# Performance work log

Measured on AMD Instinct MI355X. Metric: run time of the kernel, lower is better.

## Reference

```python
import jax, jax.numpy as jnp
import numpy as np

B, S, D, H = 2, 2048, 2048, 16
HD = D // H  # head_dim = 128


def setup_inputs() -> dict:
    key = jax.random.key(0)
    ks = jax.random.split(key, 5)
    scale = 1.0 / np.sqrt(D)
    return {
        "x": jax.random.normal(ks[0], (B, S, D), dtype=jnp.float32),
        "wq": jax.random.normal(ks[1], (D, D), dtype=jnp.float32) * scale,
        "wk": jax.random.normal(ks[2], (D, D), dtype=jnp.float32) * scale,
        "wv": jax.random.normal(ks[3], (D, D), dtype=jnp.float32) * scale,
        "wo": jax.random.normal(ks[4], (D, D), dtype=jnp.float32) * scale,
        "bo": jnp.zeros((D,), dtype=jnp.float32),
    }


def reference(x, wq, wk, wv, wo, bo):
    b, s, _ = x.shape
    # torch Linear: y = x @ W.T ; then view(b,s,H,HD) and transpose to (b,H,s,HD)
    q = (x @ wq.T).reshape(b, s, H, HD).transpose(0, 2, 1, 3)
    k = (x @ wk.T).reshape(b, s, H, HD).transpose(0, 2, 1, 3)
    v = (x @ wv.T).reshape(b, s, H, HD).transpose(0, 2, 1, 3)
    scores = jnp.einsum("bhqd,bhkd->bhqk", q, k)
    causal = jnp.triu(jnp.ones((s, s), dtype=bool), k=1)  # True above diagonal
    scores = jnp.where(causal[None, None], -jnp.inf, scores)
    attn = jax.nn.softmax(scores / np.sqrt(HD), axis=-1)
    # dropout p=0.0 -> identity
    ctx = jnp.einsum("bhqk,bhkd->bhqd", attn, v)
    ctx = ctx.transpose(0, 2, 1, 3).reshape(b, s, D)
    return ctx @ wo.T + bo
```

## Files before the change

kernel.cpp:

```cpp
#include <hip/hip_runtime.h>
#include <math.h>

typedef __bf16 bf16_t;
typedef __bf16 bf16x8 __attribute__((ext_vector_type(8)));
typedef float f32x4 __attribute__((ext_vector_type(4)));

__device__ __forceinline__ void gload_lds16(const bf16_t* g, bf16_t* l) {
    __builtin_amdgcn_global_load_lds((const __attribute__((address_space(1))) void*)g,
                                     (__attribute__((address_space(3))) void*)l, 16, 0, 0);
}

__global__ __launch_bounds__(256) void cvt_all(const float* __restrict__ x,
                                               const float* __restrict__ wq,
                                               const float* __restrict__ wk,
                                               const float* __restrict__ wv,
                                               const float* __restrict__ wo,
                                               bf16_t* __restrict__ dst) {
    int c = blockIdx.x * 256 + threadIdx.x;
    const float* src;
    size_t off;
    if (c < 1048576) { src = x; off = c; }
    else {
        int q = (c - 1048576) >> 19;
        src = (q == 0) ? wq : (q == 1) ? wk : (q == 2) ? wv : wo;
        off = (c - 1048576) & 524287;
    }
    const float4* p = (const float4*)src + off * 2;
    float4 a = p[0], b = p[1];
    union { bf16_t h[8]; uint4 u; } pk;
    pk.h[0] = (bf16_t)a.x; pk.h[1] = (bf16_t)a.y; pk.h[2] = (bf16_t)a.z; pk.h[3] = (bf16_t)a.w;
    pk.h[4] = (bf16_t)b.x; pk.h[5] = (bf16_t)b.y; pk.h[6] = (bf16_t)b.z; pk.h[7] = (bf16_t)b.w;
    ((uint4*)dst)[c] = pk.u;
}

template <int MODE, typename OutT>
__device__ __forceinline__ void gemm_core(bf16_t* __restrict__ AsB, bf16_t* __restrict__ BsB,
                                          const bf16_t* __restrict__ A,
                                          const bf16_t* __restrict__ Bm,
                                          const float* __restrict__ bias,
                                          OutT* __restrict__ C, bf16_t* __restrict__ Vt,
                                          int M, int N, int K, int bx, int by) {
    const int tid = threadIdx.x;
    const int w = tid >> 6, l = tid & 63;
    const int l16 = l & 15, lg = l >> 4;
    const int wr = w >> 1, wc = w & 1;
    const int m0 = bx * 256, n0 = by * 128;
    const int lsw = l16 & 7;

    f32x4 acc[4][4] = {};

    auto stageA = [&](int k0, int buf) {
#pragma unroll
        for (int j = 0; j < 4; ++j) {
            int c = tid + j * 512;
            int row = c >> 3;
            int kc = (c & 7) ^ (row & 7);
            gload_lds16(A + (size_t)(m0 + row) * K + k0 + kc * 8,
                        &AsB[buf * 16384 + (j * 512 + w * 64) * 8]);
        }
    };
    auto stageB = [&](int k0, int buf) {
#pragma unroll
        for (int j = 0; j < 2; ++j) {
            int c = tid + j * 512;
            int row = c >> 3;
            int kc = (c & 7) ^ (row & 7);
            gload_lds16(Bm + (size_t)(n0 + row) * K + k0 + kc * 8,
                        &BsB[buf * 8192 + (j * 512 + w * 64) * 8]);
        }
    };

    stageA(0, 0); stageB(0, 0);
    stageA(64, 1); stageB(64, 1);
    asm volatile("s_waitcnt vmcnt(6)" ::: "memory");
    __builtin_amdgcn_s_barrier();

    const int nt = K / 64;
    int cur = 0;
    for (int t = 0; t < nt; ++t) {
        int nxt = cur + 2; if (nxt >= 3) nxt -= 3;
        const bool pf = (t + 2 < nt);
        const int k2 = (t + 2) * 64;
        const bf16_t* Asc = &AsB[cur * 16384];
        const bf16_t* Bsc = &BsB[cur * 8192];

        bf16x8 bfr[4][2], af[2][2];
#pragma unroll
        for (int nf = 0; nf < 4; ++nf)
#pragma unroll
            for (int ks = 0; ks < 2; ++ks) {
                int brow = wc * 64 + nf * 16 + l16;
                bfr[nf][ks] = *(const bf16x8*)&Bsc[brow * 64 + (((ks << 2) | lg) ^ lsw) * 8];
            }
#pragma unroll
        for (int i = 0; i < 2; ++i)
#pragma unroll
            for (int ks = 0; ks < 2; ++ks) {
                int arow = wr * 64 + i * 16 + l16;
                af[i][ks] = *(const bf16x8*)&Asc[arow * 64 + (((ks << 2) | lg) ^ lsw) * 8];
            }
        if (pf) stageA(k2, nxt);
        asm volatile("s_waitcnt lgkmcnt(0)" ::: "memory");
        __builtin_amdgcn_sched_barrier(0);
        __builtin_amdgcn_s_setprio(1);
#pragma unroll
        for (int ks = 0; ks < 2; ++ks)
#pragma unroll
            for (int i = 0; i < 2; ++i)
#pragma unroll
                for (int nf = 0; nf < 4; ++nf)
                    acc[i][nf] = __builtin_amdgcn_mfma_f32_16x16x32_bf16(af[i][ks], bfr[nf][ks], acc[i][nf], 0, 0, 0);
        __builtin_amdgcn_s_setprio(0);

        bf16x8 af2[2][2];
#pragma unroll
        for (int i = 0; i < 2; ++i)
#pragma unroll
            for (int ks = 0; ks < 2; ++ks) {
                int arow = wr * 64 + (i + 2) * 16 + l16;
                af2[i][ks] = *(const bf16x8*)&Asc[arow * 64 + (((ks << 2) | lg) ^ lsw) * 8];
            }
        if (pf) stageB(k2, nxt);
        asm volatile("s_waitcnt lgkmcnt(0)" ::: "memory");
        __builtin_amdgcn_sched_barrier(0);
        __builtin_amdgcn_s_setprio(1);
#pragma unroll
        for (int ks = 0; ks < 2; ++ks)
#pragma unroll
            for (int i = 0; i < 2; ++i)
#pragma unroll
                for (int nf = 0; nf < 4; ++nf)
                    acc[i + 2][nf] = __builtin_amdgcn_mfma_f32_16x16x32_bf16(af2[i][ks], bfr[nf][ks], acc[i + 2][nf], 0, 0, 0);
        __builtin_amdgcn_s_setprio(0);

        if (pf) asm volatile("s_waitcnt vmcnt(6)" ::: "memory");
        else    asm volatile("s_waitcnt vmcnt(0)" ::: "memory");
        __builtin_amdgcn_s_barrier();
        cur = (cur + 1 == 3) ? 0 : cur + 1;
    }

    if constexpr (MODE == 2) {
#pragma unroll
        for (int mf = 0; mf < 4; ++mf)
#pragma unroll
            for (int nf = 0; nf < 4; ++nf) {
                int col = n0 + wc * 64 + nf * 16 + l16;
                int hh = col >> 7, dh = col & 127;
                int rowbase = m0 + wr * 64 + mf * 16 + lg * 4;
                int bb = rowbase >> 11, s = rowbase & 2047;
                union { bf16_t h[4]; ushort4 u4; } pk;
#pragma unroll
                for (int r = 0; r < 4; ++r) pk.h[r] = (bf16_t)acc[mf][nf][r];
                *(ushort4*)&Vt[(((size_t)(bb * 16 + hh)) * 128 + dh) * 2048 + s] = pk.u4;
            }
    } else {
#pragma unroll
        for (int mf = 0; mf < 4; ++mf)
#pragma unroll
            for (int nf = 0; nf < 4; ++nf) {
                int col = n0 + wc * 64 + nf * 16 + l16;
                float bv = (MODE == 1) ? bias[col] : 0.f;
#pragma unroll
                for (int r = 0; r < 4; ++r) {
                    int row = m0 + wr * 64 + mf * 16 + lg * 4 + r;
                    C[(size_t)row * N + col] = (OutT)(acc[mf][nf][r] + bv);
                }
            }
    }
}

__global__ __launch_bounds__(512, 2) void gemm_qkv(const bf16_t* __restrict__ A,
                                                   const bf16_t* __restrict__ W0,
                                                   const bf16_t* __restrict__ W1,
                                                   const bf16_t* __restrict__ W2,
                                                   bf16_t* __restrict__ O0, bf16_t* __restrict__ O1,
                                                   bf16_t* __restrict__ Vt, int M, int N, int K) {
    __shared__ __align__(16) bf16_t As[3 * 256 * 64];
    __shared__ __align__(16) bf16_t Bs[3 * 128 * 64];
    int flat = blockIdx.x + 16 * (blockIdx.y + 16 * blockIdx.z);
    int idx = (flat & 7) * 96 + (flat >> 3);
    int bx = idx & 15, by = (idx >> 4) & 15, bz = idx >> 8;
    if (bz == 0)      gemm_core<0, bf16_t>(As, Bs, A, W0, nullptr, O0, nullptr, M, N, K, bx, by);
    else if (bz == 1) gemm_core<0, bf16_t>(As, Bs, A, W1, nullptr, O1, nullptr, M, N, K, bx, by);
    else              gemm_core<2, bf16_t>(As, Bs, A, W2, nullptr, (bf16_t*)nullptr, Vt, M, N, K, bx, by);
}

__global__ __launch_bounds__(512, 2) void gemm_bias_f32(const bf16_t* __restrict__ A,
                                                        const bf16_t* __restrict__ Bm,
                                                        const float* __restrict__ bias,
                                                        float* __restrict__ C, int M, int N, int K) {
    __shared__ __align__(16) bf16_t As[3 * 256 * 64];
    __shared__ __align__(16) bf16_t Bs[3 * 128 * 64];
    int flat = blockIdx.x + 16 * blockIdx.y;
    int idx = (flat & 7) * 32 + (flat >> 3);
    int bx = idx & 15, by = idx >> 4;
    gemm_core<1, float>(As, Bs, A, Bm, bias, C, nullptr, M, N, K, bx, by);
}

__global__ __launch_bounds__(512) void attn_fwd(const bf16_t* __restrict__ Q,
                                                const bf16_t* __restrict__ Kk,
                                                const bf16_t* __restrict__ Vt,
                                                bf16_t* __restrict__ Ctx, int S, int H) {
    const int D = H * 128;
    const int p = blockIdx.x;
    const int bh = blockIdx.y;
    const int b = bh >> 4, h = bh & 15;
    const int tid = threadIdx.x;
    const int w = tid >> 6, l = tid & 63;
    const int l16 = l & 15, lg = l >> 4;

    __shared__ __align__(16) bf16_t ks[2][64 * 128];
    __shared__ __align__(16) bf16_t vs[2][64 * 128];
    __shared__ __align__(16) bf16_t ps[8][16 * 64];

    const float scale = 0.08838834764831845f;
    const f32x4 zero4 = {0.f, 0.f, 0.f, 0.f};

    auto stage = [&](int k0, int buf) {
#pragma unroll
        for (int j = 0; j < 2; ++j) {
            int c = tid + j * 512;
            int r = c >> 4;
            int c8 = (c & 15) ^ (r & 7);
            gload_lds16(Kk + (size_t)(b * S + k0 + r) * D + h * 128 + c8 * 8,
                        &ks[buf][(w * 64 + j * 512) * 8]);
            int dd = c >> 3;
            int k8 = (c & 7) ^ (dd & 7);
            gload_lds16(Vt + ((size_t)bh * 128 + dd) * S + k0 + k8 * 8,
                        &vs[buf][(w * 64 + j * 512) * 8]);
        }
    };

    for (int job = 0; job < 2; ++job) {
        const int qt = job ? (15 - p) : p;
        const int q0 = qt * 128;
        const int nkt = 2 * qt + 2;
        const int rmin = q0 + w * 16, rmax = rmin + 15;

        bf16x8 qf[4];
        {
            const bf16_t* qp = Q + (size_t)(b * S + rmin + l16) * D + h * 128 + lg * 8;
#pragma unroll
            for (int d4 = 0; d4 < 4; ++d4) qf[d4] = *(const bf16x8*)(qp + d4 * 32);
        }
        f32x4 ctx[8];
#pragma unroll
        for (int f = 0; f < 8; ++f) ctx[f] = zero4;
        float mrun[4] = {-INFINITY, -INFINITY, -INFINITY, -INFINITY};
        float lrun[4] = {0.f, 0.f, 0.f, 0.f};

        __syncthreads();
        stage(0, 0);
        int cur = 0;
        for (int kt = 0; kt < nkt; ++kt) {
            __syncthreads();
            if (kt + 1 < nkt) stage((kt + 1) * 64, cur ^ 1);
            const int k0 = kt * 64;
            if (k0 <= rmax) {
                f32x4 sacc[4];
#pragma unroll
                for (int kc = 0; kc < 4; ++kc) sacc[kc] = zero4;
#pragma unroll
                for (int kc = 0; kc < 4; ++kc) {
                    const int krow = kc * 16 + l16;
#pragma unroll
                    for (int d4 = 0; d4 < 4; ++d4) {
                        bf16x8 kf = *(const bf16x8*)&ks[cur][(krow * 16 + ((d4 * 4 + lg) ^ (krow & 7))) * 8];
                        sacc[kc] = __builtin_amdgcn_mfma_f32_16x16x32_bf16(qf[d4], kf, sacc[kc], 0, 0, 0);
                    }
                }
                float sv[4][4];
                const bool needmask = (k0 + 63 > rmin);
#pragma unroll
                for (int kc = 0; kc < 4; ++kc)
#pragma unroll
                    for (int r = 0; r < 4; ++r) {
                        float s = sacc[kc][r] * scale;
                        if (needmask && (k0 + kc * 16 + l16) > (rmin + lg * 4 + r)) s = -INFINITY;
                        sv[kc][r] = s;
                    }
                float alpha[4];
#pragma unroll
                for (int r = 0; r < 4; ++r) {
                    float mx = fmaxf(fmaxf(sv[0][r], sv[1][r]), fmaxf(sv[2][r], sv[3][r]));
#pragma unroll
                    for (int off = 1; off < 16; off <<= 1) mx = fmaxf(mx, __shfl_xor(mx, off));
                    float mnew = fmaxf(mrun[r], mx);
                    alpha[r] = (mrun[r] == -INFINITY) ? 0.f : __expf(mrun[r] - mnew);
                    float psum = 0.f;
#pragma unroll
                    for (int kc = 0; kc < 4; ++kc) {
                        float pe = __expf(sv[kc][r] - mnew);
                        sv[kc][r] = pe;
                        psum += pe;
                    }
#pragma unroll
                    for (int off = 1; off < 16; off <<= 1) psum += __shfl_xor(psum, off);
                    lrun[r] = lrun[r] * alpha[r] + psum;
                    mrun[r] = mnew;
                }
#pragma unroll
                for (int f = 0; f < 8; ++f) {
                    ctx[f][0] *= alpha[0]; ctx[f][1] *= alpha[1];
                    ctx[f][2] *= alpha[2]; ctx[f][3] *= alpha[3];
                }
#pragma unroll
                for (int r = 0; r < 4; ++r) {
                    int prow = lg * 4 + r;
#pragma unroll
                    for (int kc = 0; kc < 4; ++kc)
                        ps[w][prow * 64 + ((kc * 16 + l16) ^ ((prow & 7) << 3))] = (bf16_t)sv[kc][r];
                }
#pragma unroll
                for (int t = 0; t < 2; ++t) {
                    bf16x8 pa = *(const bf16x8*)&ps[w][l16 * 64 + ((t * 32 + lg * 8) ^ ((l16 & 7) << 3))];
#pragma unroll
                    for (int f = 0; f < 8; ++f) {
                        bf16x8 vb = *(const bf16x8*)&vs[cur][((f * 16 + l16) * 8 + ((t * 4 + lg) ^ (l16 & 7))) * 8];
                        ctx[f] = __builtin_amdgcn_mfma_f32_16x16x32_bf16(pa, vb, ctx[f], 0, 0, 0);
                    }
                }
            }
            cur ^= 1;
        }
        float invl[4];
#pragma unroll
        for (int r = 0; r < 4; ++r) invl[r] = 1.f / lrun[r];
#pragma unroll
        for (int f = 0; f < 8; ++f)
#pragma unroll
            for (int r = 0; r < 4; ++r) {
                int qrow = rmin + lg * 4 + r;
                Ctx[(size_t)(b * S + qrow) * D + h * 128 + f * 16 + l16] = (bf16_t)(ctx[f][r] * invl[r]);
            }
    }
}

extern "C" void kernel_launch(void* const* d_in, const int* in_sizes, int n_in,
                              void* d_out, int out_size, void* d_ws, size_t ws_size,
                              hipStream_t stream) {
    const int B = 2, S = 2048, D = 2048, H = 16;
    const int M = B * S;
    const float* x  = (const float*)d_in[0];
    const float* wq = (const float*)d_in[1];
    const float* wk = (const float*)d_in[2];
    const float* wv = (const float*)d_in[3];
    const float* wo = (const float*)d_in[4];
    const float* bo = (const float*)d_in[5];
    float* out = (float*)d_out;

    char* ws = (char*)d_ws;
    const size_t MB = 1024 * 1024;
    if (ws_size < 128 * MB) return;
    bf16_t* xb  = (bf16_t*)(ws);
    bf16_t* wqb = (bf16_t*)(ws + 16 * MB);
    bf16_t* wkb = (bf16_t*)(ws + 24 * MB);
    bf16_t* wvb = (bf16_t*)(ws + 32 * MB);
    bf16_t* wob = (bf16_t*)(ws + 40 * MB);
    bf16_t* qb  = (bf16_t*)(ws + 48 * MB);
    bf16_t* kb  = (bf16_t*)(ws + 64 * MB);
    bf16_t* vtb = (bf16_t*)(ws + 80 * MB);
    bf16_t* cxb = (bf16_t*)(ws + 96 * MB);

    cvt_all<<<12288, 256, 0, stream>>>(x, wq, wk, wv, wo, xb);
    gemm_qkv<<<dim3(16, 16, 3), 512, 0, stream>>>(xb, wqb, wkb, wvb, qb, kb, vtb, M, D, D);
    attn_fwd<<<dim3(8, B * H), 512, 0, stream>>>(qb, kb, vtb, cxb, S, H);
    gemm_bias_f32<<<dim3(16, 16), 512, 0, stream>>>(cxb, wob, bo, out, M, D, D);
}
```

Measured before the change: 278.4 us.

## Rewrite attention with 32x32 MFMA, register-resident P and lazy rescaling

Reworks the flash attention kernel to use 32x32x16 MFMA with transposed S = K·Q^T, so each lane owns one query row. P is passed to the PV matmul through cross-lane shuffles instead of an LDS round trip, exp2 replaces exp with the log2e folded into the scale, and the running-max rescale is skipped unless the max grows by more than a threshold. The grid changes to 256-row query blocks without the paired-tile load balancing, with launch bounds asking for two blocks per CU. This drops LDS traffic and softmax overhead, but the causal work per block becomes uneven and register pressure rises.

Result: faster. 270.7 us (-2.8%).

```diff
diff --git a/kernel.cpp b/kernel.cpp
--- a/kernel.cpp
+++ b/kernel.cpp
@@ -4,6 +4,7 @@
 typedef __bf16 bf16_t;
 typedef __bf16 bf16x8 __attribute__((ext_vector_type(8)));
 typedef float f32x4 __attribute__((ext_vector_type(4)));
+typedef float f32x16 __attribute__((ext_vector_type(16)));
 
 __device__ __forceinline__ void gload_lds16(const bf16_t* g, bf16_t* l) {
     __builtin_amdgcn_global_load_lds((const __attribute__((address_space(1))) void*)g,
@@ -197,143 +198,154 @@
     gemm_core<1, float>(As, Bs, A, Bm, bias, C, nullptr, M, N, K, bx, by);
 }
 
-__global__ __launch_bounds__(512) void attn_fwd(const bf16_t* __restrict__ Q,
-                                                const bf16_t* __restrict__ Kk,
-                                                const bf16_t* __restrict__ Vt,
-                                                bf16_t* __restrict__ Ctx, int S, int H) {
+__global__ __launch_bounds__(512, 2) void attn_fwd(const bf16_t* __restrict__ Q,
+                                                   const bf16_t* __restrict__ Kk,
+                                                   const bf16_t* __restrict__ Vt,
+                                                   bf16_t* __restrict__ Ctx, int S, int H) {
     const int D = H * 128;
-    const int p = blockIdx.x;
-    const int bh = blockIdx.y;
+    const int bh = blockIdx.x;
+    const int qb = blockIdx.y;
     const int b = bh >> 4, h = bh & 15;
     const int tid = threadIdx.x;
     const int w = tid >> 6, l = tid & 63;
-    const int l16 = l & 15, lg = l >> 4;
+    const int l32 = l & 31, hi = l >> 5;
+    const int q0w = qb * 256 + w * 32;
+    const int qrow = q0w + l32;
 
     __shared__ __align__(16) bf16_t ks[2][64 * 128];
-    __shared__ __align__(16) bf16_t vs[2][64 * 128];
-    __shared__ __align__(16) bf16_t ps[8][16 * 64];
-
-    const float scale = 0.08838834764831845f;
-    const f32x4 zero4 = {0.f, 0.f, 0.f, 0.f};
+    __shared__ __align__(16) bf16_t vs[2][128 * 64];
+
+    bf16x8 qf[8];
+    {
+        const bf16_t* qp = Q + (size_t)(b * S + qrow) * D + h * 128 + hi * 8;
+#pragma unroll
+        for (int d = 0; d < 8; ++d) qf[d] = *(const bf16x8*)(qp + d * 16);
+    }
+
+    f32x16 ctx[4] = {};
+    float mrun = -INFINITY, lrun = 0.f;
+    const float Cs = 0.08838834764831845f * 1.4426950408889634f;
 
     auto stage = [&](int k0, int buf) {
 #pragma unroll
         for (int j = 0; j < 2; ++j) {
             int c = tid + j * 512;
             int r = c >> 4;
-            int c8 = (c & 15) ^ (r & 7);
-            gload_lds16(Kk + (size_t)(b * S + k0 + r) * D + h * 128 + c8 * 8,
-                        &ks[buf][(w * 64 + j * 512) * 8]);
+            int c16 = (c & 15) ^ (r & 7);
+            gload_lds16(Kk + (size_t)(b * S + k0 + r) * D + h * 128 + c16 * 8,
+                        &ks[buf][(j * 512 + w * 64) * 8]);
             int dd = c >> 3;
             int k8 = (c & 7) ^ (dd & 7);
             gload_lds16(Vt + ((size_t)bh * 128 + dd) * S + k0 + k8 * 8,
-                        &vs[buf][(w * 64 + j * 512) * 8]);
+                        &vs[buf][(j * 512 + w * 64) * 8]);
         }
     };
 
-    for (int job = 0; job < 2; ++job) {
-        const int qt = job ? (15 - p) : p;
-        const int q0 = qt * 128;
-        const int nkt = 2 * qt + 2;
-        const int rmin = q0 + w * 16, rmax = rmin + 15;
-
-        bf16x8 qf[4];
-        {
-            const bf16_t* qp = Q + (size_t)(b * S + rmin + l16) * D + h * 128 + lg * 8;
-#pragma unroll
-            for (int d4 = 0; d4 < 4; ++d4) qf[d4] = *(const bf16x8*)(qp + d4 * 32);
-        }
-        f32x4 ctx[8];
-#pragma unroll
-        for (int f = 0; f < 8; ++f) ctx[f] = zero4;
-        float mrun[4] = {-INFINITY, -INFINITY, -INFINITY, -INFINITY};
-        float lrun[4] = {0.f, 0.f, 0.f, 0.f};
-
+    stage(0, 0);
+    const int nkt = 4 * qb + 4;
+    int cur = 0;
+    for (int kt = 0; kt < nkt; ++kt) {
         __syncthreads();
-        stage(0, 0);
-        int cur = 0;
-        for (int kt = 0; kt < nkt; ++kt) {
-            __syncthreads();
-            if (kt + 1 < nkt) stage((kt + 1) * 64, cur ^ 1);
-            const int k0 = kt * 64;
-            if (k0 <= rmax) {
-                f32x4 sacc[4];
-#pragma unroll
-                for (int kc = 0; kc < 4; ++kc) sacc[kc] = zero4;
-#pragma unroll
-                for (int kc = 0; kc < 4; ++kc) {
-                    const int krow = kc * 16 + l16;
-#pragma unroll
-                    for (int d4 = 0; d4 < 4; ++d4) {
-                        bf16x8 kf = *(const bf16x8*)&ks[cur][(krow * 16 + ((d4 * 4 + lg) ^ (krow & 7))) * 8];
-                        sacc[kc] = __builtin_amdgcn_mfma_f32_16x16x32_bf16(qf[d4], kf, sacc[kc], 0, 0, 0);
+        if (kt + 1 < nkt) stage((kt + 1) * 64, cur ^ 1);
+        const int k0 = kt * 64;
+        if (k0 <= q0w + 31) {
+            f32x16 sacc[2] = {};
+#pragma unroll
+            for (int d = 0; d < 8; ++d) {
+#pragma unroll
+                for (int t2 = 0; t2 < 2; ++t2) {
+                    int row = t2 * 32 + l32;
+                    int c16 = (2 * d + hi) ^ (row & 7);
+                    bf16x8 kf = *(const bf16x8*)&ks[cur][(row * 16 + c16) * 8];
+                    sacc[t2] = __builtin_amdgcn_mfma_f32_32x32x16_bf16(kf, qf[d], sacc[t2], 0, 0, 0);
+                }
+            }
+            const bool diag = (k0 + 63 > q0w);
+#pragma unroll
+            for (int t2 = 0; t2 < 2; ++t2)
+#pragma unroll
+                for (int c = 0; c < 16; ++c) {
+                    float s = sacc[t2][c] * Cs;
+                    if (diag) {
+                        int key = k0 + 32 * t2 + (c & 3) + 8 * (c >> 2) + 4 * hi;
+                        if (key > qrow) s = -INFINITY;
                     }
-                }
-                float sv[4][4];
-                const bool needmask = (k0 + 63 > rmin);
-#pragma unroll
-                for (int kc = 0; kc < 4; ++kc)
-#pragma unroll
-                    for (int r = 0; r < 4; ++r) {
-                        float s = sacc[kc][r] * scale;
-                        if (needmask && (k0 + kc * 16 + l16) > (rmin + lg * 4 + r)) s = -INFINITY;
-                        sv[kc][r] = s;
-                    }
-                float alpha[4];
-#pragma unroll
-                for (int r = 0; r < 4; ++r) {
-                    float mx = fmaxf(fmaxf(sv[0][r], sv[1][r]), fmaxf(sv[2][r], sv[3][r]));
-#pragma unroll
-                    for (int off = 1; off < 16; off <<= 1) mx = fmaxf(mx, __shfl_xor(mx, off));
-                    float mnew = fmaxf(mrun[r], mx);
-                    alpha[r] = (mrun[r] == -INFINITY) ? 0.f : __expf(mrun[r] - mnew);
-                    float psum = 0.f;
-#pragma unroll
-                    for (int kc = 0; kc < 4; ++kc) {
-                        float pe = __expf(sv[kc][r] - mnew);
-                        sv[kc][r] = pe;
-                        psum += pe;
-                    }
-#pragma unroll
-                    for (int off = 1; off < 16; off <<= 1) psum += __shfl_xor(psum, off);
-                    lrun[r] = lrun[r] * alpha[r] + psum;
-                    mrun[r] = mnew;
-                }
-#pragma unroll
-                for (int f = 0; f < 8; ++f) {
-                    ctx[f][0] *= alpha[0]; ctx[f][1] *= alpha[1];
-                    ctx[f][2] *= alpha[2]; ctx[f][3] *= alpha[3];
-                }
-#pragma unroll
-                for (int r = 0; r < 4; ++r) {
-                    int prow = lg * 4 + r;
-#pragma unroll
-                    for (int kc = 0; kc < 4; ++kc)
-                        ps[w][prow * 64 + ((kc * 16 + l16) ^ ((prow & 7) << 3))] = (bf16_t)sv[kc][r];
-                }
-#pragma unroll
-                for (int t = 0; t < 2; ++t) {
-                    bf16x8 pa = *(const bf16x8*)&ps[w][l16 * 64 + ((t * 32 + lg * 8) ^ ((l16 & 7) << 3))];
-#pragma unroll
-                    for (int f = 0; f < 8; ++f) {
-                        bf16x8 vb = *(const bf16x8*)&vs[cur][((f * 16 + l16) * 8 + ((t * 4 + lg) ^ (l16 & 7))) * 8];
-                        ctx[f] = __builtin_amdgcn_mfma_f32_16x16x32_bf16(pa, vb, ctx[f], 0, 0, 0);
-                    }
-                }
-            }
-            cur ^= 1;
-        }
-        float invl[4];
-#pragma unroll
-        for (int r = 0; r < 4; ++r) invl[r] = 1.f / lrun[r];
-#pragma unroll
-        for (int f = 0; f < 8; ++f)
-#pragma unroll
-            for (int r = 0; r < 4; ++r) {
-                int qrow = rmin + lg * 4 + r;
-                Ctx[(size_t)(b * S + qrow) * D + h * 128 + f * 16 + l16] = (bf16_t)(ctx[f][r] * invl[r]);
-            }
-    }
+                    sacc[t2][c] = s;
+                }
+            float tm[16];
+#pragma unroll
+            for (int c = 0; c < 16; ++c) tm[c] = fmaxf(sacc[0][c], sacc[1][c]);
+#pragma unroll
+            for (int sft = 8; sft; sft >>= 1)
+#pragma unroll
+                for (int c = 0; c < 8; ++c)
+                    if (c < sft) tm[c] = fmaxf(tm[c], tm[c + sft]);
+            float pmax = fmaxf(tm[0], __shfl_xor(tm[0], 32));
+            if (!__all(pmax <= mrun + 8.f)) {
+                float mnew = fmaxf(mrun, pmax);
+                float alpha = exp2f(mrun - mnew);
+                lrun *= alpha;
+#pragma unroll
+                for (int dblk = 0; dblk < 4; ++dblk)
+#pragma unroll
+                    for (int c = 0; c < 16; ++c) ctx[dblk][c] *= alpha;
+                mrun = mnew;
+            }
+#pragma unroll
+            for (int t2 = 0; t2 < 2; ++t2)
+#pragma unroll
+                for (int c = 0; c < 16; ++c) sacc[t2][c] = exp2f(sacc[t2][c] - mrun);
+            float ts[16];
+#pragma unroll
+            for (int c = 0; c < 16; ++c) ts[c] = sacc[0][c] + sacc[1][c];
+#pragma unroll
+            for (int sft = 8; sft; sft >>= 1)
+#pragma unroll
+                for (int c = 0; c < 8; ++c)
+                    if (c < sft) ts[c] += ts[c + sft];
+            lrun += ts[0] + __shfl_xor(ts[0], 32);
+            bf16x8 pa[4];
+#pragma unroll
+            for (int ksx = 0; ksx < 4; ++ksx) {
+                const int t2 = ksx >> 1, cb = (ksx & 1) * 8;
+                union { bf16_t hh[4]; unsigned u[2]; } Wlo, Whi;
+#pragma unroll
+                for (int i = 0; i < 4; ++i) {
+                    Wlo.hh[i] = (bf16_t)sacc[t2][cb + i];
+                    Whi.hh[i] = (bf16_t)sacc[t2][cb + 4 + i];
+                }
+                unsigned s0 = hi ? Wlo.u[0] : Whi.u[0];
+                unsigned s1 = hi ? Wlo.u[1] : Whi.u[1];
+                unsigned r0 = __shfl_xor(s0, 32);
+                unsigned r1 = __shfl_xor(s1, 32);
+                union { unsigned u[4]; bf16x8 v; } F;
+                if (hi == 0) { F.u[0] = Wlo.u[0]; F.u[1] = Wlo.u[1]; F.u[2] = r0; F.u[3] = r1; }
+                else         { F.u[0] = r0; F.u[1] = r1; F.u[2] = Whi.u[0]; F.u[3] = Whi.u[1]; }
+                pa[ksx] = F.v;
+            }
+#pragma unroll
+            for (int ksx = 0; ksx < 4; ++ksx)
+#pragma unroll
+                for (int dblk = 0; dblk < 4; ++dblk) {
+                    int dd = dblk * 32 + l32;
+                    int k8 = (2 * ksx + hi) ^ (dd & 7);
+                    bf16x8 vf = *(const bf16x8*)&vs[cur][(dd * 8 + k8) * 8];
+                    ctx[dblk] = __builtin_amdgcn_mfma_f32_32x32x16_bf16(vf, pa[ksx], ctx[dblk], 0, 0, 0);
+                }
+        }
+        cur ^= 1;
+    }
+    float invl = 1.f / lrun;
+    bf16_t* op = Ctx + (size_t)(b * S + qrow) * D + h * 128;
+#pragma unroll
+    for (int dblk = 0; dblk < 4; ++dblk)
+#pragma unroll
+        for (int cg = 0; cg < 4; ++cg) {
+            union { bf16_t hh[4]; ushort4 u4; } pk;
+#pragma unroll
+            for (int i = 0; i < 4; ++i) pk.hh[i] = (bf16_t)(ctx[dblk][cg * 4 + i] * invl);
+            *(ushort4*)&op[dblk * 32 + cg * 8 + hi * 4] = pk.u4;
+        }
 }
 
 extern "C" void kernel_launch(void* const* d_in, const int* in_sizes, int n_in,
@@ -364,6 +376,6 @@
 
     cvt_all<<<12288, 256, 0, stream>>>(x, wq, wk, wv, wo, xb);
     gemm_qkv<<<dim3(16, 16, 3), 512, 0, stream>>>(xb, wqb, wkb, wvb, qb, kb, vtb, M, D, D);
-    attn_fwd<<<dim3(8, B * H), 512, 0, stream>>>(qb, kb, vtb, cxb, S, H);
+    attn_fwd<<<dim3(32, 8), 512, 0, stream>>>(qb, kb, vtb, cxb, S, H);
     gemm_bias_f32<<<dim3(16, 16), 512, 0, stream>>>(cxb, wob, bo, out, M, D, D);
 }
```
